# Optimization experiments

Hardware: AMD Instinct MI355X
Metric: run time of the kernel (lower is better)

Reference implementation:

```python
import jax, jax.numpy as jnp
import numpy as np

ALIGNED = 7            # aligned_height == aligned_width
GRID = ALIGNED + 1     # RoIAlignFunction samples an 8x8 grid


def _roi_align_grid(features, rois, scale):
    """jwyang-style RoIAlign: one bilinear sample per grid point.
    features: [B, C, H, W]; rois: [N, 5] = (batch_idx, x1, y1, x2, y2) in image coords.
    Returns [N, C, GRID, GRID].
    """
    B, C, H, W = features.shape
    b = rois[:, 0].astype(jnp.int32)                      # [N]
    x1, y1, x2, y2 = (rois[:, i] * scale for i in (1, 2, 3, 4))
    roi_w = jnp.maximum(x2 - x1, 0.0)
    roi_h = jnp.maximum(y2 - y1, 0.0)
    bin_h = roi_h / (GRID - 1)
    bin_w = roi_w / (GRID - 1)

    g = jnp.arange(GRID, dtype=features.dtype)
    ys = y1[:, None] + g * bin_h[:, None]                 # [N, GRID]
    xs = x1[:, None] + g * bin_w[:, None]                 # [N, GRID]

    valid = ((ys >= 0) & (ys < H))[:, :, None] & ((xs >= 0) & (xs < W))[:, None, :]  # [N,G,G]

    y0 = jnp.clip(jnp.floor(ys), 0, H - 2).astype(jnp.int32)  # [N, GRID]
    x0 = jnp.clip(jnp.floor(xs), 0, W - 2).astype(jnp.int32)
    ly = (ys - y0)[:, :, None]                            # [N, GRID, 1]
    lx = (xs - x0)[:, None, :]                            # [N, 1, GRID]

    bi = b[:, None, None]                                 # [N,1,1]
    yy0, yy1 = y0[:, :, None], y0[:, :, None] + 1          # [N,GRID,1]
    xx0, xx1 = x0[:, None, :], x0[:, None, :] + 1          # [N,1,GRID]

    # Each gather -> [N, GRID, GRID, C]
    v00 = features[bi, :, yy0, xx0]
    v01 = features[bi, :, yy0, xx1]
    v10 = features[bi, :, yy1, xx0]
    v11 = features[bi, :, yy1, xx1]

    wy0, wy1 = (1.0 - ly)[..., None], ly[..., None]        # [N,GRID,1,1]
    wx0, wx1 = (1.0 - lx)[..., None], lx[..., None]        # [N,1,GRID,1]
    val = wy0 * (wx0 * v00 + wx1 * v01) + wy1 * (wx0 * v10 + wx1 * v11)
    val = jnp.where(valid[..., None], val, 0.0)            # [N,GRID,GRID,C]
    return jnp.transpose(val, (0, 3, 1, 2))                # [N,C,GRID,GRID]


def _avg_pool2x2_s1(x):
    return 0.25 * (x[..., :-1, :-1] + x[..., :-1, 1:] + x[..., 1:, :-1] + x[..., 1:, 1:])


def setup_inputs() -> dict:
    key = jax.random.key(0)
    k1, k2, k3, k4, k5 = jax.random.split(key, 5)
    B, C, H, W = 2, 256, 100, 100
    N = 2048
    img = 1600.0  # image size; feature = img * scale
    features = jax.random.normal(k1, (B, C, H, W), dtype=jnp.float32)
    bidx = jax.random.randint(k2, (N,), 0, B).astype(jnp.float32)
    xy1 = jax.random.uniform(k3, (N, 2), minval=0.0, maxval=img - 64.0)
    wh = jax.random.uniform(k4, (N, 2), minval=16.0, maxval=400.0)
    xy2 = jnp.minimum(xy1 + wh, img - 1.0)
    rois = jnp.concatenate([bidx[:, None], xy1[:, :1], xy1[:, 1:], xy2[:, :1], xy2[:, 1:]], axis=1)
    return {"features": features, "rois": rois.astype(jnp.float32), "scale": jnp.float32(0.0625)}


def reference(features, rois, scale):
    x = _roi_align_grid(features, rois, scale)   # [N, C, 8, 8]
    return _avg_pool2x2_s1(x)                    # [N, C, 7, 7]
```

## Files before the change

### kernel.cpp

```cpp
#include <hip/hip_runtime.h>
#include <hip/hip_bf16.h>
#include <stdint.h>

#define FB 2
#define FC 256
#define FH 100
#define FW 100
#define HW (FH * FW)
#define OUTHW 49
#define OUT_PER_ROI (FC * OUTHW)
#define CHUNK 64
#define NCHUNK (FC / CHUNK)

typedef unsigned int uint4v __attribute__((ext_vector_type(4)));
typedef float float2v __attribute__((ext_vector_type(2)));

__global__ __launch_bounds__(256) void transpose_chw_hwc(
    const float* __restrict__ in, __hip_bfloat16* __restrict__ out) {
  __shared__ float tile[32][33];
  const int b  = blockIdx.z;
  const int c0 = blockIdx.y * 32;
  const int p0 = blockIdx.x * 32;
  const int tx = threadIdx.x;
  const int ty = threadIdx.y;
  const int p = p0 + tx;
  if (p < HW) {
#pragma unroll
    for (int cy = ty; cy < 32; cy += 8) {
      tile[cy][tx] = in[(size_t)(b * FC + c0 + cy) * HW + p];
    }
  }
  __syncthreads();
#pragma unroll
  for (int py = ty; py < 32; py += 8) {
    const int pp = p0 + py;
    if (pp < HW) {
      out[(size_t)(b * HW + pp) * FC + c0 + tx] = __float2bfloat16(tile[tx][py]);
    }
  }
}

__global__ __launch_bounds__(256) void roialign_avg_kernel(
    const __hip_bfloat16* __restrict__ F,
    const float* __restrict__ rois,
    const float* __restrict__ scale_p,
    float* __restrict__ out) {
  __shared__ float s_s[8][8][CHUNK];
  __shared__ __align__(16) float s_o[CHUNK * OUTHW];

  const int n     = blockIdx.x;
  const int chunk = blockIdx.y;
  const int tid   = threadIdx.x;
  const int c2 = tid & 31;
  const int r  = tid >> 5;

  const float scale = scale_p[0];
  const int   bi = (int)rois[n * 5 + 0];
  const float x1 = rois[n * 5 + 1] * scale;
  const float y1 = rois[n * 5 + 2] * scale;
  const float x2 = rois[n * 5 + 3] * scale;
  const float y2 = rois[n * 5 + 4] * scale;
  const float bin_w = fmaxf(x2 - x1, 0.0f) / 7.0f;
  const float bin_h = fmaxf(y2 - y1, 0.0f) / 7.0f;

  const float ysf = y1 + (float)r * bin_h;
  const bool  vy = (ysf >= 0.0f) && (ysf < (float)FH);
  const int   y0 = (int)fminf(fmaxf(floorf(ysf), 0.0f), (float)(FH - 2));
  const float ly = ysf - (float)y0;
  const float wy0 = 1.0f - ly, wy1 = ly;
  const int rowbase = (bi * HW + y0 * FW) * FC + chunk * CHUNK + 2 * c2;
  const uint32_t* __restrict__ Fu =
      reinterpret_cast<const uint32_t*>(F);

  float samp0[8], samp1[8];
#pragma unroll
  for (int gx = 0; gx < 8; ++gx) {
    const float xsf = x1 + (float)gx * bin_w;
    const bool  v = vy && (xsf >= 0.0f) && (xsf < (float)FW);
    const int   x0 = (int)fminf(fmaxf(floorf(xsf), 0.0f), (float)(FW - 2));
    const float lx = xsf - (float)x0;
    const float w00 = v ? wy0 * (1.0f - lx) : 0.0f;
    const float w01 = v ? wy0 * lx          : 0.0f;
    const float w10 = v ? wy1 * (1.0f - lx) : 0.0f;
    const float w11 = v ? wy1 * lx          : 0.0f;
    const int o = (rowbase + x0 * FC) >> 1;
    const uint32_t u00 = Fu[o];
    const uint32_t u01 = Fu[o + FC / 2];
    const uint32_t u10 = Fu[o + (FW * FC) / 2];
    const uint32_t u11 = Fu[o + (FW * FC) / 2 + FC / 2];
    const float a00 = __uint_as_float(u00 << 16), b00 = __uint_as_float(u00 & 0xffff0000u);
    const float a01 = __uint_as_float(u01 << 16), b01 = __uint_as_float(u01 & 0xffff0000u);
    const float a10 = __uint_as_float(u10 << 16), b10 = __uint_as_float(u10 & 0xffff0000u);
    const float a11 = __uint_as_float(u11 << 16), b11 = __uint_as_float(u11 & 0xffff0000u);
    samp0[gx] = w00 * a00 + w01 * a01 + w10 * a10 + w11 * a11;
    samp1[gx] = w00 * b00 + w01 * b01 + w10 * b10 + w11 * b11;
  }
#pragma unroll
  for (int gx = 0; gx < 8; ++gx) {
    float2v* p = reinterpret_cast<float2v*>(&s_s[r][gx][2 * c2]);
    float2v v2; v2.x = samp0[gx]; v2.y = samp1[gx];
    *p = v2;
  }
  __syncthreads();

  {
    const int c = tid & 63;
    const int r0 = tid >> 6;
#pragma unroll
    for (int rp = r0; rp < 7; rp += 4) {
      float a[8];
#pragma unroll
      for (int j = 0; j < 8; ++j) a[j] = s_s[rp][j][c] + s_s[rp + 1][j][c];
      float* so = s_o + c * OUTHW + rp * 7;
#pragma unroll
      for (int j = 0; j < 7; ++j) so[j] = 0.25f * (a[j] + a[j + 1]);
    }
  }
  __syncthreads();

  const uint4v* src = (const uint4v*)s_o;
  uint4v* dst = (uint4v*)(out + (size_t)n * OUT_PER_ROI + chunk * (CHUNK * OUTHW));
#pragma unroll
  for (int k = tid; k < (CHUNK * OUTHW) / 4; k += 256) {
    __builtin_nontemporal_store(src[k], &dst[k]);
  }
}

extern "C" void kernel_launch(void* const* d_in, const int* in_sizes, int n_in,
                              void* d_out, int out_size, void* d_ws, size_t ws_size,
                              hipStream_t stream) {
  const float* features = (const float*)d_in[0];
  const float* rois     = (const float*)d_in[1];
  const float* scale    = (const float*)d_in[2];
  float* out = (float*)d_out;
  __hip_bfloat16* ft = (__hip_bfloat16*)d_ws;

  const int N = in_sizes[1] / 5;

  dim3 tb(32, 8);
  dim3 tg((HW + 31) / 32, FC / 32, FB);
  transpose_chw_hwc<<<tg, tb, 0, stream>>>(features, ft);

  roialign_avg_kernel<<<dim3(N, NCHUNK), dim3(256), 0, stream>>>(ft, rois, scale, out);
}
```

Baseline: 141.1 us.

## Widen RoIAlign per-thread channels to 4 and fuse horizontal pooling in registers

```diff
diff --git a/kernel.cpp b/kernel.cpp
--- a/kernel.cpp
+++ b/kernel.cpp
@@ -13,20 +13,28 @@
 #define NCHUNK (FC / CHUNK)
 
 typedef unsigned int uint4v __attribute__((ext_vector_type(4)));
-typedef float float2v __attribute__((ext_vector_type(2)));
+typedef unsigned int uint2v __attribute__((ext_vector_type(2)));
+typedef float float4v __attribute__((ext_vector_type(4)));
+
+#define LOF(u) __uint_as_float((u) << 16)
+#define HIF(u) __uint_as_float((u) & 0xffff0000u)
+
+static __device__ __forceinline__ uint16_t f32_to_bf16_bits(float x) {
+  return __builtin_bit_cast(uint16_t, __float2bfloat16(x));
+}
 
 __global__ __launch_bounds__(256) void transpose_chw_hwc(
-    const float* __restrict__ in, __hip_bfloat16* __restrict__ out) {
-  __shared__ float tile[32][33];
+    const float* __restrict__ in, uint32_t* __restrict__ out) {
+  __shared__ float tile[64][33];
   const int b  = blockIdx.z;
-  const int c0 = blockIdx.y * 32;
+  const int c0 = blockIdx.y * 64;
   const int p0 = blockIdx.x * 32;
   const int tx = threadIdx.x;
   const int ty = threadIdx.y;
   const int p = p0 + tx;
   if (p < HW) {
 #pragma unroll
-    for (int cy = ty; cy < 32; cy += 8) {
+    for (int cy = ty; cy < 64; cy += 8) {
       tile[cy][tx] = in[(size_t)(b * FC + c0 + cy) * HW + p];
     }
   }
@@ -35,24 +43,26 @@
   for (int py = ty; py < 32; py += 8) {
     const int pp = p0 + py;
     if (pp < HW) {
-      out[(size_t)(b * HW + pp) * FC + c0 + tx] = __float2bfloat16(tile[tx][py]);
+      const uint32_t lo = f32_to_bf16_bits(tile[2 * tx][py]);
+      const uint32_t hi = f32_to_bf16_bits(tile[2 * tx + 1][py]);
+      out[((size_t)(b * HW + pp) * FC + c0) / 2 + tx] = (hi << 16) | lo;
     }
   }
 }
 
-__global__ __launch_bounds__(256) void roialign_avg_kernel(
+__global__ __launch_bounds__(128) void roialign_avg_kernel(
     const __hip_bfloat16* __restrict__ F,
     const float* __restrict__ rois,
     const float* __restrict__ scale_p,
     float* __restrict__ out) {
-  __shared__ float s_s[8][8][CHUNK];
+  __shared__ float s_h[7][7][CHUNK];
   __shared__ __align__(16) float s_o[CHUNK * OUTHW];
 
   const int n     = blockIdx.x;
   const int chunk = blockIdx.y;
   const int tid   = threadIdx.x;
-  const int c2 = tid & 31;
-  const int r  = tid >> 5;
+  const int c4 = tid & 15;
+  const int r  = tid >> 4;
 
   const float scale = scale_p[0];
   const int   bi = (int)rois[n * 5 + 0];
@@ -60,19 +70,20 @@
   const float y1 = rois[n * 5 + 2] * scale;
   const float x2 = rois[n * 5 + 3] * scale;
   const float y2 = rois[n * 5 + 4] * scale;
-  const float bin_w = fmaxf(x2 - x1, 0.0f) / 7.0f;
-  const float bin_h = fmaxf(y2 - y1, 0.0f) / 7.0f;
+  const float bin_w = fmaxf(x2 - x1, 0.0f) * (1.0f / 7.0f);
+  const float bin_h = fmaxf(y2 - y1, 0.0f) * (1.0f / 7.0f);
 
   const float ysf = y1 + (float)r * bin_h;
   const bool  vy = (ysf >= 0.0f) && (ysf < (float)FH);
   const int   y0 = (int)fminf(fmaxf(floorf(ysf), 0.0f), (float)(FH - 2));
   const float ly = ysf - (float)y0;
   const float wy0 = 1.0f - ly, wy1 = ly;
-  const int rowbase = (bi * HW + y0 * FW) * FC + chunk * CHUNK + 2 * c2;
-  const uint32_t* __restrict__ Fu =
-      reinterpret_cast<const uint32_t*>(F);
+  const int rowbase = (bi * HW + y0 * FW) * FC + chunk * CHUNK + 4 * c4;
+  const uint2v* __restrict__ Fu =
+      reinterpret_cast<const uint2v*>(F);
 
-  float samp0[8], samp1[8];
+  float h[4][7];
+  float prev[4] = {0.0f, 0.0f, 0.0f, 0.0f};
 #pragma unroll
   for (int gx = 0; gx < 8; ++gx) {
     const float xsf = x1 + (float)gx * bin_w;
@@ -83,45 +94,50 @@
     const float w01 = v ? wy0 * lx          : 0.0f;
     const float w10 = v ? wy1 * (1.0f - lx) : 0.0f;
     const float w11 = v ? wy1 * lx          : 0.0f;
-    const int o = (rowbase + x0 * FC) >> 1;
-    const uint32_t u00 = Fu[o];
-    const uint32_t u01 = Fu[o + FC / 2];
-    const uint32_t u10 = Fu[o + (FW * FC) / 2];
-    const uint32_t u11 = Fu[o + (FW * FC) / 2 + FC / 2];
-    const float a00 = __uint_as_float(u00 << 16), b00 = __uint_as_float(u00 & 0xffff0000u);
-    const float a01 = __uint_as_float(u01 << 16), b01 = __uint_as_float(u01 & 0xffff0000u);
-    const float a10 = __uint_as_float(u10 << 16), b10 = __uint_as_float(u10 & 0xffff0000u);
-    const float a11 = __uint_as_float(u11 << 16), b11 = __uint_as_float(u11 & 0xffff0000u);
-    samp0[gx] = w00 * a00 + w01 * a01 + w10 * a10 + w11 * a11;
-    samp1[gx] = w00 * b00 + w01 * b01 + w10 * b10 + w11 * b11;
+    const int o = (rowbase + x0 * FC) >> 2;
+    const uint2v u00 = Fu[o];
+    const uint2v u01 = Fu[o + FC / 4];
+    const uint2v u10 = Fu[o + (FW * FC) / 4];
+    const uint2v u11 = Fu[o + (FW * FC) / 4 + FC / 4];
+    float s[4];
+    s[0] = w00 * LOF(u00.x) + w01 * LOF(u01.x) + w10 * LOF(u10.x) + w11 * LOF(u11.x);
+    s[1] = w00 * HIF(u00.x) + w01 * HIF(u01.x) + w10 * HIF(u10.x) + w11 * HIF(u11.x);
+    s[2] = w00 * LOF(u00.y) + w01 * LOF(u01.y) + w10 * LOF(u10.y) + w11 * LOF(u11.y);
+    s[3] = w00 * HIF(u00.y) + w01 * HIF(u01.y) + w10 * HIF(u10.y) + w11 * HIF(u11.y);
+    if (gx > 0) {
+#pragma unroll
+      for (int cc = 0; cc < 4; ++cc) h[cc][gx - 1] = prev[cc] + s[cc];
+    }
+#pragma unroll
+    for (int cc = 0; cc < 4; ++cc) prev[cc] = s[cc];
   }
+
+  if (r > 0) {
 #pragma unroll
-  for (int gx = 0; gx < 8; ++gx) {
-    float2v* p = reinterpret_cast<float2v*>(&s_s[r][gx][2 * c2]);
-    float2v v2; v2.x = samp0[gx]; v2.y = samp1[gx];
-    *p = v2;
+    for (int j = 0; j < 7; ++j) {
+      float4v v4;
+      v4.x = h[0][j]; v4.y = h[1][j]; v4.z = h[2][j]; v4.w = h[3][j];
+      *reinterpret_cast<float4v*>(&s_h[r - 1][j][4 * c4]) = v4;
+    }
   }
   __syncthreads();
 
-  {
-    const int c = tid & 63;
-    const int r0 = tid >> 6;
+  if (r < 7) {
+    float* b = s_o + (4 * c4) * OUTHW + r * 7;
 #pragma unroll
-    for (int rp = r0; rp < 7; rp += 4) {
-      float a[8];
-#pragma unroll
-      for (int j = 0; j < 8; ++j) a[j] = s_s[rp][j][c] + s_s[rp + 1][j][c];
-      float* so = s_o + c * OUTHW + rp * 7;
-#pragma unroll
-      for (int j = 0; j < 7; ++j) so[j] = 0.25f * (a[j] + a[j + 1]);
+    for (int j = 0; j < 7; ++j) {
+      const float4v v4 = *reinterpret_cast<const float4v*>(&s_h[r][j][4 * c4]);
+      b[j]              = 0.25f * (h[0][j] + v4.x);
+      b[OUTHW + j]      = 0.25f * (h[1][j] + v4.y);
+      b[2 * OUTHW + j]  = 0.25f * (h[2][j] + v4.z);
+      b[3 * OUTHW + j]  = 0.25f * (h[3][j] + v4.w);
     }
   }
   __syncthreads();
 
   const uint4v* src = (const uint4v*)s_o;
   uint4v* dst = (uint4v*)(out + (size_t)n * OUT_PER_ROI + chunk * (CHUNK * OUTHW));
-#pragma unroll
-  for (int k = tid; k < (CHUNK * OUTHW) / 4; k += 256) {
+  for (int k = tid; k < (CHUNK * OUTHW) / 4; k += 128) {
     __builtin_nontemporal_store(src[k], &dst[k]);
   }
 }
@@ -138,8 +154,8 @@
   const int N = in_sizes[1] / 5;
 
   dim3 tb(32, 8);
-  dim3 tg((HW + 31) / 32, FC / 32, FB);
-  transpose_chw_hwc<<<tg, tb, 0, stream>>>(features, ft);
+  dim3 tg((HW + 31) / 32, FC / 64, FB);
+  transpose_chw_hwc<<<tg, tb, 0, stream>>>(features, (uint32_t*)ft);
 
-  roialign_avg_kernel<<<dim3(N, NCHUNK), dim3(256), 0, stream>>>(ft, rois, scale, out);
+  roialign_avg_kernel<<<dim3(N, NCHUNK), dim3(128), 0, stream>>>(ft, rois, scale, out);
 }
```

Result: no change. 143.3 us (+1.6%).
